# Optimization experiments

Measured on AMD Instinct MI355X. Metric: run time of the kernel, lower is better.

Reference implementation:

```python
import jax, jax.numpy as jnp
import numpy as np

N_VOX = 200_000
C = 64
B, G = 2, 128  # batch size, grid resolution per axis
K = 27         # 3x3x3 kernel volume
EPS = 1e-5


def _build_coords_and_kernel_map(seed=0):
    """Build unique voxel coords on a [B,G,G,G] grid and the 27-offset kernel map.

    nbr[i, k] = row index of the voxel at coord[i] + offset[k], or N_VOX if absent
    (sentinel row that gathers zeros). This mirrors MinkowskiEngine's
    coordinate-hash in/out kernel maps for a stride-1 conv.
    """
    rng = np.random.default_rng(seed)
    total = B * G * G * G
    keys = np.sort(rng.choice(total, size=N_VOX, replace=False).astype(np.int64))
    z = keys % G
    y = (keys // G) % G
    x = (keys // (G * G)) % G
    b = keys // (G * G * G)
    offs = [(dx, dy, dz) for dx in (-1, 0, 1) for dy in (-1, 0, 1) for dz in (-1, 0, 1)]
    nbr = np.full((N_VOX, K), N_VOX, dtype=np.int64)
    for k, (dx, dy, dz) in enumerate(offs):
        nx, ny, nz = x + dx, y + dy, z + dz
        valid = (nx >= 0) & (nx < G) & (ny >= 0) & (ny < G) & (nz >= 0) & (nz < G)
        nkey = ((b * G + nx) * G + ny) * G + nz
        pos = np.clip(np.searchsorted(keys, nkey), 0, N_VOX - 1)
        found = valid & (keys[pos] == nkey)
        nbr[:, k] = np.where(found, pos, N_VOX)
    return jnp.asarray(nbr)


def setup_inputs() -> dict:
    key = jax.random.key(0)
    ks = jax.random.split(key, 12)
    w_scale = 1.0 / np.sqrt(K * C)
    inp = {
        "feats": jax.random.normal(ks[0], (N_VOX, C), jnp.float32),
        "nbr": _build_coords_and_kernel_map(),
        "W1": jax.random.normal(ks[1], (K, C, C), jnp.float32) * w_scale,
        "g1": 1.0 + 0.1 * jax.random.normal(ks[2], (C,), jnp.float32),
        "b1": 0.1 * jax.random.normal(ks[3], (C,), jnp.float32),
        "m1": 0.1 * jax.random.normal(ks[4], (C,), jnp.float32),
        "v1": jax.random.uniform(ks[5], (C,), jnp.float32, 0.5, 1.5),
        "W2": jax.random.normal(ks[6], (K, C, C), jnp.float32) * w_scale,
        "g2": 1.0 + 0.1 * jax.random.normal(ks[7], (C,), jnp.float32),
        "b2": 0.1 * jax.random.normal(ks[8], (C,), jnp.float32),
        "m2": 0.1 * jax.random.normal(ks[9], (C,), jnp.float32),
        "v2": jax.random.uniform(ks[10], (C,), jnp.float32, 0.5, 1.5),
    }
    return inp


def _bn(x, g, b, m, v):
    # MinkowskiBatchNorm, eval mode: per-channel affine with running stats
    return (x - m) * (g * jax.lax.rsqrt(v + EPS)) + b


def _sparse_conv(feats, nbr, W):
    # gather-GEMM-scatter sparse 3D conv over the precomputed kernel map.
    # Sentinel index N_VOX gathers the appended zero row (missing neighbor).
    fpad = jnp.concatenate([feats, jnp.zeros((1, feats.shape[1]), feats.dtype)], axis=0)
    out = jnp.zeros((feats.shape[0], W.shape[2]), feats.dtype)
    for k in range(W.shape[0]):  # fixed 27-tap loop (structural, not data dim)
        out = out + fpad[nbr[:, k]] @ W[k]
    return out


def reference(feats, nbr, W1, g1, b1, m1, v1, W2, g2, b2, m2, v2):
    h = jax.nn.relu(_bn(_sparse_conv(feats, nbr, W1), g1, b1, m1, v1))
    h = _bn(_sparse_conv(h, nbr, W2), g2, b2, m2, v2)
    # in_channels == out_channels and stride == 1 -> identity shortcut
    return jax.nn.relu(h + feats)
```

## Files before the change

### kernel.cpp

```cpp
#include <hip/hip_runtime.h>
#include <hip/hip_bf16.h>

#define NVOX 200000
#define NTAP 27
#define OSTR 68
#define ROWB 128

typedef __bf16          bf16x8 __attribute__((ext_vector_type(8)));
typedef unsigned short  u16x8  __attribute__((ext_vector_type(8)));
typedef float           f32x4  __attribute__((ext_vector_type(4)));

#define FB_BYTES    ((size_t)(NVOX + 1) * ROWB)
#define WSHUF_BYTES (NTAP * 2 * 4 * 64 * 16)
#define FB_OFF      0
#define H_OFF       (FB_BYTES)
#define WS1_OFF     (2 * FB_BYTES)
#define WS2_OFF     (WS1_OFF + WSHUF_BYTES)
#define FLAG_OFF    (WS2_OFF + WSHUF_BYTES)

static __device__ __forceinline__ unsigned short f2bf_bits(float f) {
    __hip_bfloat16 h = __float2bfloat16(f);
    union { __hip_bfloat16 h; unsigned short u; } u; u.h = h; return u.u;
}
static __device__ __forceinline__ float bf2f(unsigned short s) {
    union { float f; unsigned u; } u; u.u = ((unsigned)s) << 16; return u.f;
}
static __device__ __forceinline__ float ld_param(const void* p, int c, int isbf) {
    return isbf ? bf2f(((const unsigned short*)p)[c]) : ((const float*)p)[c];
}
static __device__ __forceinline__ void gload_lds16(const void* gp, void* lp) {
    __builtin_amdgcn_global_load_lds(
        (const __attribute__((address_space(1))) void*)gp,
        (__attribute__((address_space(3))) void*)lp, 16, 0, 0);
}
static __device__ __forceinline__ int wave_isbf(const unsigned* v1w) {
    int l = threadIdx.x & 63;
    int ok = 1;
    if (l < 32) {
        unsigned w = v1w[l], lo = w & 0xFFFFu, hi = w >> 16;
        ok = (lo >= 0x3F00u && lo <= 0x3FC0u && hi >= 0x3F00u && hi <= 0x3FC0u);
    }
    return __all(ok);
}

__global__ __launch_bounds__(256)
void prep_kernel(const void* __restrict__ feats,
                 const void* __restrict__ W1, const void* __restrict__ W2,
                 const unsigned* __restrict__ v1w, const unsigned* __restrict__ nbrw,
                 uint4* __restrict__ fbuf, uint4* __restrict__ hbuf,
                 uint4* __restrict__ Ws1, uint4* __restrict__ Ws2,
                 int* __restrict__ flags) {
    const int bx = blockIdx.x;
    if (bx < 6250) {
        const int isbf = wave_isbf(v1w);
        size_t t = (size_t)bx * 256 + threadIdx.x;
        if (isbf) {
            fbuf[t] = ((const uint4*)feats)[t];
        } else {
            float4 a = ((const float4*)feats)[2 * t];
            float4 b = ((const float4*)feats)[2 * t + 1];
            union { uint4 q; unsigned short u[8]; } o;
            o.u[0] = f2bf_bits(a.x); o.u[1] = f2bf_bits(a.y);
            o.u[2] = f2bf_bits(a.z); o.u[3] = f2bf_bits(a.w);
            o.u[4] = f2bf_bits(b.x); o.u[5] = f2bf_bits(b.y);
            o.u[6] = f2bf_bits(b.z); o.u[7] = f2bf_bits(b.w);
            fbuf[t] = o.q;
        }
    } else if (bx < 6358) {
        const int isbf = wave_isbf(v1w);
        int t = (bx - 6250) * 256 + threadIdx.x;
        const void* W = (t < 13824) ? W1 : W2;
        uint4* Ws     = (t < 13824) ? Ws1 : Ws2;
        int f = (t < 13824) ? t : t - 13824;
        int k  = f / 512;
        int r  = f % 512;
        int kc = r / 256;
        int r2 = r % 256;
        int nc = r2 / 64;
        int l  = r2 % 64;
        int quad = l >> 4, li = l & 15;
        unsigned short tmp[8];
#pragma unroll
        for (int j = 0; j < 8; ++j) {
            int off = k * 4096 + (kc * 32 + quad * 8 + j) * 64 + (nc * 16 + li);
            tmp[j] = isbf ? ((const unsigned short*)W)[off]
                          : f2bf_bits(((const float*)W)[off]);
        }
        uint4 v;
        v.x = (unsigned)tmp[0] | ((unsigned)tmp[1] << 16);
        v.y = (unsigned)tmp[2] | ((unsigned)tmp[3] << 16);
        v.z = (unsigned)tmp[4] | ((unsigned)tmp[5] << 16);
        v.w = (unsigned)tmp[6] | ((unsigned)tmp[7] << 16);
        Ws[f] = v;
    } else {
        int t = threadIdx.x;
        if (t < 64) {
            int isbf = wave_isbf(v1w);
            int n64ok = 1;
#pragma unroll
            for (int i = 0; i < 8; ++i)
                if (nbrw[2 * (t * 8 + i) + 1] != 0u) n64ok = 0;
            int n64 = __all(n64ok);
            if (t == 0) { flags[0] = isbf; flags[1] = n64; }
        }
        uint4 z = make_uint4(0u, 0u, 0u, 0u);
        if (t >= 64 && t < 72) fbuf[(size_t)NVOX * 8 + (t - 64)] = z;
        if (t >= 72 && t < 80) hbuf[(size_t)NVOX * 8 + (t - 72)] = z;
    }
}

#define STG(kk, bp) do {                                                    \
    if ((mgw >> (kk)) & 1) {                                                \
        int ia_ = nbrG[o0 + (kk) * tmul];                                   \
        int ib_ = nbrG[o1 + (kk) * tmul];                                   \
        gload_lds16(srcB + (size_t)ia_ * ROWB + f0 * 16,                    \
                    (void*)((bp) + w * 128));                               \
        gload_lds16(srcB + (size_t)ib_ * ROWB + f1 * 16,                    \
                    (void*)((bp) + w * 128 + 64));                         \
    } } while (0)

#define LOADB(kk, B0r, B1r) do {                                            \
    B0r = Ws[(kk) * 512 + w * 64 + l];                                      \
    B1r = Ws[(kk) * 512 + 256 + w * 64 + l];                                \
} while (0)

#define COMPUTE(kk, bp, B0, B1) do {                                        \
    _Pragma("unroll")                                                       \
    for (int g = 0; g < 4; ++g) {                                           \
        if ((mg[g] >> (kk)) & 1) {                                          \
            bf16x8 a0_ = *(const bf16x8*)((bp) + ro0[g]);                   \
            bf16x8 a1_ = *(const bf16x8*)((bp) + ro1[g]);                   \
            acc[g] = __builtin_amdgcn_mfma_f32_16x16x32_bf16(a0_, B0, acc[g], 0, 0, 0); \
            acc[g] = __builtin_amdgcn_mfma_f32_16x16x32_bf16(a1_, B1, acc[g], 0, 0, 0); \
        }                                                                   \
    }                                                                       \
} while (0)

__global__ __launch_bounds__(256, 8)
void conv_bn_kernel(const uint4* __restrict__ srcV,
                    const void* __restrict__ nbr,
                    const bf16x8* __restrict__ Ws,
                    const void* __restrict__ gg, const void* __restrict__ bb,
                    const void* __restrict__ mm, const void* __restrict__ vv,
                    const u16x8* __restrict__ resid,
                    const int* __restrict__ flags,
                    void* __restrict__ dst, int final_out) {
    __shared__ __align__(16) int smi[64 * OSTR];
    int*   maskLDS = smi;
    uint4* at0     = (uint4*)(smi + 4);
    uint4* at1     = at0 + 512;
    float* outLDS  = (float*)smi;

    const int tid  = threadIdx.x;
    const int nwg  = gridDim.x;
    const int orig = blockIdx.x;
    const int qq   = nwg >> 3, rr = nwg & 7;
    const int xcd  = orig & 7, idx = orig >> 3;
    const int bid  = (xcd < rr ? xcd * (qq + 1) : rr * (qq + 1) + (xcd - rr) * qq) + idx;
    const int base = bid * 64;

    const int isbf = flags[0];
    const int n64  = flags[1];
    const char* srcB = (const char*)srcV;

    const int* nbrG = (const int*)nbr;
    const int  tmul = n64 ? 2 : 1;
    const int  smul = NTAP * tmul;

    if (tid < 4) maskLDS[tid] = 0;
    __syncthreads();

    if (tid < NTAP * 4) {
        int k = tid >> 2, g = tid & 3;
        int ofs = (base + g * 16) * smul + k * tmul;
        int mn = 0x7fffffff;
#pragma unroll
        for (int r = 0; r < 16; ++r) mn = min(mn, nbrG[ofs + r * smul]);
        if (mn < NVOX) atomicOr(&maskLDS[g], 1 << k);
    }
    __syncthreads();

    const int w = tid >> 6, l = tid & 63;
    const int quad = l >> 4, li = l & 15;

    int mg[4];
#pragma unroll
    for (int g = 0; g < 4; ++g) mg[g] = __builtin_amdgcn_readfirstlane(maskLDS[g]);
    const int mgw = __builtin_amdgcn_readfirstlane(maskLDS[w]);

    const int s0 = w * 128 + l;
    const int s1 = s0 + 64;
    const int r0 = s0 >> 3, f0 = (s0 - r0) & 7;
    const int r1 = s1 >> 3, f1 = (s1 - r1) & 7;
    const int o0 = (base + r0) * smul;
    const int o1 = (base + r1) * smul;
    int ro0[4], ro1[4];
#pragma unroll
    for (int g = 0; g < 4; ++g) {
        int row = g * 16 + li;
        ro0[g] = row * 8 + ((quad + row) & 7);
        ro1[g] = row * 8 + ((quad + 4 + row) & 7);
    }

    f32x4 acc[4];
#pragma unroll
    for (int g = 0; g < 4; ++g) acc[g] = (f32x4){0.f, 0.f, 0.f, 0.f};

    bf16x8 xB0, xB1, yB0, yB1;

    STG(0, at0);
    LOADB(0, xB0, xB1);
    __syncthreads();

    for (int k = 0; k < 26; k += 2) {
        STG(k + 1, at1);
        LOADB(k + 1, yB0, yB1);
        COMPUTE(k, at0, xB0, xB1);
        __syncthreads();
        STG(k + 2, at0);
        LOADB(k + 2, xB0, xB1);
        COMPUTE(k + 1, at1, yB0, yB1);
        __syncthreads();
    }
    COMPUTE(26, at0, xB0, xB1);

    const int c = w * 16 + li;
    float scale = ld_param(gg, c, isbf) * rsqrtf(ld_param(vv, c, isbf) + 1e-5f);
    float offs  = ld_param(bb, c, isbf) - ld_param(mm, c, isbf) * scale;

    __syncthreads();
#pragma unroll
    for (int g = 0; g < 4; ++g)
#pragma unroll
        for (int r = 0; r < 4; ++r)
            outLDS[(g * 16 + quad * 4 + r) * OSTR + c] = acc[g][r] * scale + offs;
    __syncthreads();

    {
        int trow = tid >> 2, cc = tid & 3;
        long grow = base + trow;
        const float4* lp = (const float4*)&outLDS[trow * OSTR + cc * 16];
        float4 q0 = lp[0], q1 = lp[1], q2 = lp[2], q3 = lp[3];
        float vals[16] = {q0.x, q0.y, q0.z, q0.w, q1.x, q1.y, q1.z, q1.w,
                          q2.x, q2.y, q2.z, q2.w, q3.x, q3.y, q3.z, q3.w};

        if (resid) {
            const u16x8* rp = resid + grow * 8 + cc * 2;
            u16x8 r0v = rp[0], r1v = rp[1];
#pragma unroll
            for (int j = 0; j < 8; ++j) { vals[j] += bf2f(r0v[j]); vals[8 + j] += bf2f(r1v[j]); }
        }
#pragma unroll
        for (int j = 0; j < 16; ++j) vals[j] = fmaxf(vals[j], 0.f);

        const int store_bf = (!final_out) || isbf;
        if (store_bf) {
            u16x8 o0v, o1v;
#pragma unroll
            for (int j = 0; j < 8; ++j) { o0v[j] = f2bf_bits(vals[j]); o1v[j] = f2bf_bits(vals[8 + j]); }
            u16x8* dp = (u16x8*)dst + grow * 8 + cc * 2;
            dp[0] = o0v; dp[1] = o1v;
        } else {
            float4* dp = (float4*)dst + grow * 16 + cc * 4;
            dp[0] = (float4){vals[0], vals[1], vals[2], vals[3]};
            dp[1] = (float4){vals[4], vals[5], vals[6], vals[7]};
            dp[2] = (float4){vals[8], vals[9], vals[10], vals[11]};
            dp[3] = (float4){vals[12], vals[13], vals[14], vals[15]};
        }
    }
}

extern "C" void kernel_launch(void* const* d_in, const int* in_sizes, int n_in,
                              void* d_out, int out_size, void* d_ws, size_t ws_size,
                              hipStream_t stream) {
    const void* feats = d_in[0];
    const void* nbr   = d_in[1];
    const void* W1    = d_in[2];
    const void* g1    = d_in[3];
    const void* b1    = d_in[4];
    const void* m1    = d_in[5];
    const void* v1    = d_in[6];
    const void* W2    = d_in[7];
    const void* g2    = d_in[8];
    const void* b2    = d_in[9];
    const void* m2    = d_in[10];
    const void* v2    = d_in[11];

    char* ws = (char*)d_ws;
    uint4* fbuf = (uint4*)(ws + FB_OFF);
    uint4* hbuf = (uint4*)(ws + H_OFF);
    uint4* Ws1  = (uint4*)(ws + WS1_OFF);
    uint4* Ws2  = (uint4*)(ws + WS2_OFF);
    int*   flags = (int*)(ws + FLAG_OFF);

    prep_kernel<<<dim3(6359), dim3(256), 0, stream>>>(
        feats, W1, W2, (const unsigned*)v1, (const unsigned*)nbr,
        fbuf, hbuf, Ws1, Ws2, flags);

    conv_bn_kernel<<<dim3(NVOX / 64), dim3(256), 0, stream>>>(
        fbuf, nbr, (const bf16x8*)Ws1, g1, b1, m1, v1,
        nullptr, flags, hbuf, 0);

    conv_bn_kernel<<<dim3(NVOX / 64), dim3(256), 0, stream>>>(
        hbuf, nbr, (const bf16x8*)Ws2, g2, b2, m2, v2,
        (const u16x8*)fbuf, flags, d_out, 1);
}
```

Before: 241.1 us.

## Double voxels per block to 128 to reuse weight fragments across more rows

Each workgroup now processes 128 voxels instead of 64. Every wave stages four gathered row chunks per tap and runs eight MFMA row groups against the same per-tap weight fragments. This halves the number of weight loads and barriers per voxel. The cost is more registers and LDS per block, with launch bounds lowered to 4 waves/EU. It also needs tail guards, because 200000 is not a multiple of 128.

Result: slower. 285.3 us (+18.3%).

```diff
diff --git a/kernel.cpp b/kernel.cpp
--- a/kernel.cpp
+++ b/kernel.cpp
@@ -5,6 +5,7 @@
 #define NTAP 27
 #define OSTR 68
 #define ROWB 128
+#define VPB  128
 
 typedef __bf16          bf16x8 __attribute__((ext_vector_type(8)));
 typedef unsigned short  u16x8  __attribute__((ext_vector_type(8)));
@@ -110,13 +111,21 @@
 }
 
 #define STG(kk, bp) do {                                                    \
-    if ((mgw >> (kk)) & 1) {                                                \
-        int ia_ = nbrG[o0 + (kk) * tmul];                                   \
-        int ib_ = nbrG[o1 + (kk) * tmul];                                   \
+    if ((mga >> (kk)) & 1) {                                                \
+        int ia_ = bad0 ? NVOX : nbrG[o0 + (kk) * tmul];                     \
+        int ib_ = bad1 ? NVOX : nbrG[o1 + (kk) * tmul];                     \
         gload_lds16(srcB + (size_t)ia_ * ROWB + f0 * 16,                    \
-                    (void*)((bp) + w * 128));                               \
+                    (void*)((bp) + w * 256));                               \
         gload_lds16(srcB + (size_t)ib_ * ROWB + f1 * 16,                    \
-                    (void*)((bp) + w * 128 + 64));                         \
+                    (void*)((bp) + w * 256 + 64));                          \
+    }                                                                       \
+    if ((mgb >> (kk)) & 1) {                                                \
+        int ic_ = bad2 ? NVOX : nbrG[o2 + (kk) * tmul];                     \
+        int id_ = bad3 ? NVOX : nbrG[o3 + (kk) * tmul];                     \
+        gload_lds16(srcB + (size_t)ic_ * ROWB + f2 * 16,                    \
+                    (void*)((bp) + w * 256 + 128));                         \
+        gload_lds16(srcB + (size_t)id_ * ROWB + f3 * 16,                    \
+                    (void*)((bp) + w * 256 + 192));                         \
     } } while (0)
 
 #define LOADB(kk, B0r, B1r) do {                                            \
@@ -126,7 +135,7 @@
 
 #define COMPUTE(kk, bp, B0, B1) do {                                        \
     _Pragma("unroll")                                                       \
-    for (int g = 0; g < 4; ++g) {                                           \
+    for (int g = 0; g < 8; ++g) {                                           \
         if ((mg[g] >> (kk)) & 1) {                                          \
             bf16x8 a0_ = *(const bf16x8*)((bp) + ro0[g]);                   \
             bf16x8 a1_ = *(const bf16x8*)((bp) + ro1[g]);                   \
@@ -136,7 +145,7 @@
     }                                                                       \
 } while (0)
 
-__global__ __launch_bounds__(256, 8)
+__global__ __launch_bounds__(256, 4)
 void conv_bn_kernel(const uint4* __restrict__ srcV,
                     const void* __restrict__ nbr,
                     const bf16x8* __restrict__ Ws,
@@ -145,10 +154,10 @@
                     const u16x8* __restrict__ resid,
                     const int* __restrict__ flags,
                     void* __restrict__ dst, int final_out) {
-    __shared__ __align__(16) int smi[64 * OSTR];
+    __shared__ __align__(16) int smi[VPB * OSTR];
     int*   maskLDS = smi;
-    uint4* at0     = (uint4*)(smi + 4);
-    uint4* at1     = at0 + 512;
+    uint4* at0     = (uint4*)(smi + 8);
+    uint4* at1     = at0 + 1024;
     float* outLDS  = (float*)smi;
 
     const int tid  = threadIdx.x;
@@ -157,7 +166,7 @@
     const int qq   = nwg >> 3, rr = nwg & 7;
     const int xcd  = orig & 7, idx = orig >> 3;
     const int bid  = (xcd < rr ? xcd * (qq + 1) : rr * (qq + 1) + (xcd - rr) * qq) + idx;
-    const int base = bid * 64;
+    const int base = bid * VPB;
 
     const int isbf = flags[0];
     const int n64  = flags[1];
@@ -167,15 +176,20 @@
     const int  tmul = n64 ? 2 : 1;
     const int  smul = NTAP * tmul;
 
-    if (tid < 4) maskLDS[tid] = 0;
-    __syncthreads();
-
-    if (tid < NTAP * 4) {
-        int k = tid >> 2, g = tid & 3;
-        int ofs = (base + g * 16) * smul + k * tmul;
+    if (tid < 8) maskLDS[tid] = 0;
+    __syncthreads();
+
+    if (tid < NTAP * 8) {
+        int k = tid >> 3, g = tid & 7;
         int mn = 0x7fffffff;
 #pragma unroll
-        for (int r = 0; r < 16; ++r) mn = min(mn, nbrG[ofs + r * smul]);
+        for (int r = 0; r < 16; ++r) {
+            int vx = base + g * 16 + r;
+            int safe = vx < NVOX ? vx : NVOX - 1;
+            int v = nbrG[safe * smul + k * tmul];
+            if (vx >= NVOX) v = NVOX;
+            mn = min(mn, v);
+        }
         if (mn < NVOX) atomicOr(&maskLDS[g], 1 << k);
     }
     __syncthreads();
@@ -183,28 +197,37 @@
     const int w = tid >> 6, l = tid & 63;
     const int quad = l >> 4, li = l & 15;
 
-    int mg[4];
-#pragma unroll
-    for (int g = 0; g < 4; ++g) mg[g] = __builtin_amdgcn_readfirstlane(maskLDS[g]);
-    const int mgw = __builtin_amdgcn_readfirstlane(maskLDS[w]);
-
-    const int s0 = w * 128 + l;
-    const int s1 = s0 + 64;
-    const int r0 = s0 >> 3, f0 = (s0 - r0) & 7;
-    const int r1 = s1 >> 3, f1 = (s1 - r1) & 7;
-    const int o0 = (base + r0) * smul;
-    const int o1 = (base + r1) * smul;
-    int ro0[4], ro1[4];
-#pragma unroll
-    for (int g = 0; g < 4; ++g) {
+    int mg[8];
+#pragma unroll
+    for (int g = 0; g < 8; ++g) mg[g] = __builtin_amdgcn_readfirstlane(maskLDS[g]);
+    const int mga = __builtin_amdgcn_readfirstlane(maskLDS[2 * w]);
+    const int mgb = __builtin_amdgcn_readfirstlane(maskLDS[2 * w + 1]);
+
+    int o_[4], f_[4], bad_[4];
+#pragma unroll
+    for (int j = 0; j < 4; ++j) {
+        int s  = w * 256 + j * 64 + l;
+        int r  = s >> 3;
+        f_[j]  = (s - r) & 7;
+        int vx = base + r;
+        bad_[j] = vx >= NVOX;
+        o_[j]  = (bad_[j] ? NVOX - 1 : vx) * smul;
+    }
+    const int o0 = o_[0], o1 = o_[1], o2 = o_[2], o3 = o_[3];
+    const int f0 = f_[0], f1 = f_[1], f2 = f_[2], f3 = f_[3];
+    const int bad0 = bad_[0], bad1 = bad_[1], bad2 = bad_[2], bad3 = bad_[3];
+
+    int ro0[8], ro1[8];
+#pragma unroll
+    for (int g = 0; g < 8; ++g) {
         int row = g * 16 + li;
         ro0[g] = row * 8 + ((quad + row) & 7);
         ro1[g] = row * 8 + ((quad + 4 + row) & 7);
     }
 
-    f32x4 acc[4];
-#pragma unroll
-    for (int g = 0; g < 4; ++g) acc[g] = (f32x4){0.f, 0.f, 0.f, 0.f};
+    f32x4 acc[8];
+#pragma unroll
+    for (int g = 0; g < 8; ++g) acc[g] = (f32x4){0.f, 0.f, 0.f, 0.f};
 
     bf16x8 xB0, xB1, yB0, yB1;
 
@@ -230,42 +253,45 @@
 
     __syncthreads();
 #pragma unroll
-    for (int g = 0; g < 4; ++g)
+    for (int g = 0; g < 8; ++g)
 #pragma unroll
         for (int r = 0; r < 4; ++r)
             outLDS[(g * 16 + quad * 4 + r) * OSTR + c] = acc[g][r] * scale + offs;
     __syncthreads();
 
-    {
-        int trow = tid >> 2, cc = tid & 3;
+#pragma unroll
+    for (int half = 0; half < 2; ++half) {
+        int trow = half * 64 + (tid >> 2), cc = tid & 3;
         long grow = base + trow;
-        const float4* lp = (const float4*)&outLDS[trow * OSTR + cc * 16];
-        float4 q0 = lp[0], q1 = lp[1], q2 = lp[2], q3 = lp[3];
-        float vals[16] = {q0.x, q0.y, q0.z, q0.w, q1.x, q1.y, q1.z, q1.w,
-                          q2.x, q2.y, q2.z, q2.w, q3.x, q3.y, q3.z, q3.w};
-
-        if (resid) {
-            const u16x8* rp = resid + grow * 8 + cc * 2;
-            u16x8 r0v = rp[0], r1v = rp[1];
-#pragma unroll
-            for (int j = 0; j < 8; ++j) { vals[j] += bf2f(r0v[j]); vals[8 + j] += bf2f(r1v[j]); }
-        }
-#pragma unroll
-        for (int j = 0; j < 16; ++j) vals[j] = fmaxf(vals[j], 0.f);
-
-        const int store_bf = (!final_out) || isbf;
-        if (store_bf) {
-            u16x8 o0v, o1v;
-#pragma unroll
-            for (int j = 0; j < 8; ++j) { o0v[j] = f2bf_bits(vals[j]); o1v[j] = f2bf_bits(vals[8 + j]); }
-            u16x8* dp = (u16x8*)dst + grow * 8 + cc * 2;
-            dp[0] = o0v; dp[1] = o1v;
-        } else {
-            float4* dp = (float4*)dst + grow * 16 + cc * 4;
-            dp[0] = (float4){vals[0], vals[1], vals[2], vals[3]};
-            dp[1] = (float4){vals[4], vals[5], vals[6], vals[7]};
-            dp[2] = (float4){vals[8], vals[9], vals[10], vals[11]};
-            dp[3] = (float4){vals[12], vals[13], vals[14], vals[15]};
+        if (grow < NVOX) {
+            const float4* lp = (const float4*)&outLDS[trow * OSTR + cc * 16];
+            float4 q0 = lp[0], q1 = lp[1], q2 = lp[2], q3 = lp[3];
+            float vals[16] = {q0.x, q0.y, q0.z, q0.w, q1.x, q1.y, q1.z, q1.w,
+                              q2.x, q2.y, q2.z, q2.w, q3.x, q3.y, q3.z, q3.w};
+
+            if (resid) {
+                const u16x8* rp = resid + grow * 8 + cc * 2;
+                u16x8 r0v = rp[0], r1v = rp[1];
+#pragma unroll
+                for (int j = 0; j < 8; ++j) { vals[j] += bf2f(r0v[j]); vals[8 + j] += bf2f(r1v[j]); }
+            }
+#pragma unroll
+            for (int j = 0; j < 16; ++j) vals[j] = fmaxf(vals[j], 0.f);
+
+            const int store_bf = (!final_out) || isbf;
+            if (store_bf) {
+                u16x8 o0v, o1v;
+#pragma unroll
+                for (int j = 0; j < 8; ++j) { o0v[j] = f2bf_bits(vals[j]); o1v[j] = f2bf_bits(vals[8 + j]); }
+                u16x8* dp = (u16x8*)dst + grow * 8 + cc * 2;
+                dp[0] = o0v; dp[1] = o1v;
+            } else {
+                float4* dp = (float4*)dst + grow * 16 + cc * 4;
+                dp[0] = (float4){vals[0], vals[1], vals[2], vals[3]};
+                dp[1] = (float4){vals[4], vals[5], vals[6], vals[7]};
+                dp[2] = (float4){vals[8], vals[9], vals[10], vals[11]};
+                dp[3] = (float4){vals[12], vals[13], vals[14], vals[15]};
+            }
         }
     }
 }
@@ -297,11 +323,12 @@
         feats, W1, W2, (const unsigned*)v1, (const unsigned*)nbr,
         fbuf, hbuf, Ws1, Ws2, flags);
 
-    conv_bn_kernel<<<dim3(NVOX / 64), dim3(256), 0, stream>>>(
+    const int nblk = (NVOX + VPB - 1) / VPB;
+    conv_bn_kernel<<<dim3(nblk), dim3(256), 0, stream>>>(
         fbuf, nbr, (const bf16x8*)Ws1, g1, b1, m1, v1,
         nullptr, flags, hbuf, 0);
 
-    conv_bn_kernel<<<dim3(NVOX / 64), dim3(256), 0, stream>>>(
+    conv_bn_kernel<<<dim3(nblk), dim3(256), 0, stream>>>(
         hbuf, nbr, (const bf16x8*)Ws2, g2, b2, m2, v2,
         (const u16x8*)fbuf, flags, d_out, 1);
 }
```
